# Optimization experiments

Measured on AMD Instinct MI355X. Metric: run time of the kernel, lower is better.

The kernel has to match this reference:

```python
import jax, jax.numpy as jnp
import numpy as np
import math

VOCAB, EMBED, RES = 50257, 512, 2048
B, T = 64, 512
LN_EPS = 1e-5


def setup_inputs() -> dict:
    key = jax.random.key(0)
    k_x, k_e, k_r, k_w = jax.random.split(key, 4)
    x = jax.random.randint(k_x, (B, T), 0, VOCAB)
    embed_weight = jax.random.normal(k_e, (VOCAB, EMBED), dtype=jnp.float32)
    R = jax.random.normal(k_r, (RES, RES), dtype=jnp.float32) / math.sqrt(RES) / 0.9
    Win = jax.random.normal(k_w, (EMBED, RES), dtype=jnp.float32) / math.sqrt(EMBED) / 0.9
    gamma = jnp.ones((RES,), dtype=jnp.float32)
    beta = jnp.zeros((RES,), dtype=jnp.float32)
    return {"x": x, "embed_weight": embed_weight, "R": R, "Win": Win,
            "gamma": gamma, "beta": beta}


def reference(x, embed_weight, R, Win, gamma, beta):
    emb = embed_weight[x]                              # [B, T, E]
    inp = jnp.einsum('bte,er->btr', emb, Win)          # [B, T, RES]

    def step(state, u_t):                              # state: [B, RES]
        new_state = jnp.tanh(state @ R + u_t)
        return new_state, None

    state0 = jnp.zeros((x.shape[0], R.shape[0]), dtype=emb.dtype)
    state, _ = jax.lax.scan(step, state0, jnp.swapaxes(inp, 0, 1))  # scan over T

    # LayerNorm over last dim (eps=1e-5, affine)
    mu = jnp.mean(state, axis=-1, keepdims=True)
    var = jnp.mean((state - mu) ** 2, axis=-1, keepdims=True)
    normed = (state - mu) / jnp.sqrt(var + LN_EPS)
    return normed * gamma + beta
```

## Files before the change

kernel.cpp:

```cpp
#include <hip/hip_runtime.h>

#define BB 64
#define TT 512
#define EE 512
#define RR 2048
#define CPW 32
#define RPG 16
#define NWGS 256
#define FPAD 16
#define SLOT2 (BB * RR * 2)
#define GRP2  (RPG * RR * 2)
#define SPIN_CAP (1 << 20)

typedef _Float16 f16;
typedef f16 f16x8 __attribute__((ext_vector_type(8)));
typedef float f32x4 __attribute__((ext_vector_type(4)));

__device__ __forceinline__ float fast_tanh(float v) {
  float e = __expf(2.0f * v);
  return 1.0f - 2.0f / (e + 1.0f);
}

__device__ __forceinline__ void storeS(f16* p, f16 h) {
  union { f16 h; unsigned short s; } u;
  u.h = h;
  __hip_atomic_store((unsigned short*)p, u.s, __ATOMIC_RELAXED, __HIP_MEMORY_SCOPE_AGENT);
}

__device__ __forceinline__ unsigned flag_ld(const unsigned* p) {
  return __hip_atomic_load(p, __ATOMIC_RELAXED, __HIP_MEMORY_SCOPE_AGENT);
}
__device__ __forceinline__ void flag_st(unsigned* p, unsigned v) {
  __hip_atomic_store(p, v, __ATOMIC_RELAXED, __HIP_MEMORY_SCOPE_AGENT);
}

__device__ __forceinline__ void issue8(f16x8* dst, unsigned voff, const f16* sbase) {
#pragma unroll
  for (int i = 0; i < 8; ++i)
    asm volatile("global_load_dwordx4 %0, %1, %2 offset:%c3"
                 : "=v"(dst[i]) : "v"(voff), "s"(sbase), "i"(64 * i) : "memory");
}
__device__ __forceinline__ void issue2(f16x8* dst, unsigned voff, const f16* sbase) {
  asm volatile("global_load_dwordx4 %0, %1, %2"
               : "=v"(dst[0]) : "v"(voff), "s"(sbase) : "memory");
  asm volatile("global_load_dwordx4 %0, %1, %2 offset:64"
               : "=v"(dst[1]) : "v"(voff), "s"(sbase) : "memory");
}

template <int N>
__device__ __forceinline__ void wait_vm() {
  asm volatile("s_waitcnt vmcnt(%c0)" :: "i"(N) : "memory");
  __builtin_amdgcn_sched_barrier(0);
}


__global__ void prep_emb(const int* __restrict__ x, const float* __restrict__ ew,
                         f16* __restrict__ emb) {
  const int row = blockIdx.x;
  const int tok = x[row];
  const float4* src = (const float4*)(ew + (size_t)tok * EE);
  f16* dst = emb + (size_t)row * EE;
  const int i = threadIdx.x;
  float4 v = src[i];
  union { f16 h[4]; unsigned long long u; } p;
  p.h[0] = (f16)v.x; p.h[1] = (f16)v.y; p.h[2] = (f16)v.z; p.h[3] = (f16)v.w;
  ((unsigned long long*)dst)[i] = p.u;
}

__global__ void prep_winT(const float* __restrict__ Win, f16* __restrict__ WinT) {
  const int i = blockIdx.x * blockDim.x + threadIdx.x;
  if (i < EE * RR) {
    const int k = i / RR, n = i % RR;
    WinT[(size_t)n * EE + k] = (f16)Win[i];
  }
}


__launch_bounds__(512, 1)
__global__ void scan_kernel(const float* __restrict__ R, f16* __restrict__ Sh,
                            const f16* __restrict__ emb, const f16* __restrict__ WinT,
                            unsigned* __restrict__ flg) {
  __shared__ __align__(16) char ldsbuf[CPW * RR * 2 + 16 * 1040];
  f16* Rt = (f16*)ldsbuf;
  const char* RtB = (const char*)ldsbuf;

  const int wg = blockIdx.x;
  const int xcd = wg & 7;
  const int grp = xcd >> 1;
  const int cw = ((wg >> 3) << 1) | (wg & 1);
  const int nbase = cw * CPW;
  const int rbase = grp * RPG;
  const int tid = threadIdx.x;
  const int wv = tid >> 6, l = tid & 63;
  unsigned* gflags = flg + (size_t)grp * 64 * FPAD;
  unsigned* myflag = gflags + cw * FPAD;
  f16* Sg = Sh + (size_t)grp * (RPG * RR);

  __builtin_amdgcn_fence(__ATOMIC_ACQUIRE, "agent");

  const int r16 = l & 15, kb = l >> 4;
  const int mm = tid >> 5, cc = tid & 31;
  const int ntr = cc >> 4;
  const int lred = (cc & 15) | ((mm >> 2) << 4);
  const int jred = mm & 3;
  char* red = ldsbuf + CPW * RR * 2;

  {
    const int c = tid & 31, kst = tid >> 5;
    for (int k = kst; k < RR; k += 16) {
      const float v = R[(size_t)k * RR + nbase + c];
      const int idx = ((k >> 5) << 10) + ((c >> 4) << 9) +
                      (((c & 15) << 2) + ((k >> 3) & 3)) * 8 + (k & 7);
      Rt[idx] = (f16)v;
    }
  }

  f16x8 wfr[2][2];
#pragma unroll
  for (int c2 = 0; c2 < 2; ++c2)
#pragma unroll
    for (int nt = 0; nt < 2; ++nt)
      wfr[c2][nt] = *(const f16x8*)&WinT[(size_t)(nbase + nt * 16 + r16) * EE +
                                         (2 * wv + c2) * 32 + kb * 8];

  const unsigned voffE0 =
      (unsigned)((((size_t)(rbase + r16) * TT) * EE + 2 * wv * 32 + kb * 8) * 2);

  {
    f16x8 ebuf[2];
    issue2(ebuf, voffE0 , emb);
    wait_vm<0>();
    f32x4 a0 = {0.f, 0.f, 0.f, 0.f}, a1 = {0.f, 0.f, 0.f, 0.f};
#pragma unroll
    for (int c2 = 0; c2 < 2; ++c2) {
      a0 = __builtin_amdgcn_mfma_f32_16x16x32_f16(ebuf[c2], wfr[c2][0], a0, 0, 0, 0);
      a1 = __builtin_amdgcn_mfma_f32_16x16x32_f16(ebuf[c2], wfr[c2][1], a1, 0, 0, 0);
    }
    *(f32x4*)(red + (wv * 2 + 0) * 1040 + l * 16) = a0;
    *(f32x4*)(red + (wv * 2 + 1) * 1040 + l * 16) = a1;
    __syncthreads();
    float s = 0.f;
#pragma unroll
    for (int w = 0; w < 8; ++w)
      s += *(const float*)(red + (w * 2 + ntr) * 1040 + lred * 16 + jred * 4);
    storeS(&Sg[(size_t)mm * RR + nbase + cc], (f16)fast_tanh(s));
    __syncthreads();
    if (tid == 0) flag_st(myflag, 1u);
  }

  const int kblk = (wv + cw) & 7;
  const unsigned voffA = (unsigned)(((r16 * RR) + (kblk << 8) + kb * 8) * 2);
  const int bb0 = (r16 * 4 + kb) * 16;

  f16x8 abuf[8];

  for (int tau = 2; tau <= TT; ++tau) {
    const unsigned need = (unsigned)(tau - 1);

    {
      const unsigned* pp = &gflags[(size_t)(kblk * 8 + (l & 7)) * FPAD];
      unsigned fv = flag_ld(pp);
      int gd = 0;
      while (!__all(fv >= need) && ++gd < SPIN_CAP) {
        __builtin_amdgcn_s_sleep(1);
        fv = flag_ld(pp);
      }
    }

    const f16* sprev = Sh + (size_t)(tau - 2) * (BB * RR) + (size_t)grp * (RPG * RR);
    f16* snext = (f16*)((char*)Sh + (size_t)(tau - 1) * SLOT2) + (size_t)grp * (RPG * RR);

    issue8(abuf, voffA, sprev);
    f16x8 ebuf[2];
    issue2(ebuf, voffE0 + (unsigned)((tau - 1) * (EE * 2)), emb);

    f32x4 acc0 = {0.f, 0.f, 0.f, 0.f}, acc1 = {0.f, 0.f, 0.f, 0.f};
#define KSTEP(ks)                                                              \
  {                                                                            \
    const int kc = (kblk << 3) + (ks);                                         \
    f16x8 b0 = *(const f16x8*)(RtB + kc * 2048 + bb0);                         \
    f16x8 b1 = *(const f16x8*)(RtB + kc * 2048 + 1024 + bb0);                  \
    acc0 = __builtin_amdgcn_mfma_f32_16x16x32_f16(abuf[ks], b0, acc0, 0, 0, 0);\
    acc1 = __builtin_amdgcn_mfma_f32_16x16x32_f16(abuf[ks], b1, acc1, 0, 0, 0);\
  }
    wait_vm<6>();
    KSTEP(0) KSTEP(1) KSTEP(2) KSTEP(3)
    wait_vm<2>();
    KSTEP(4) KSTEP(5) KSTEP(6) KSTEP(7)
#undef KSTEP
    wait_vm<0>();
#pragma unroll
    for (int c2 = 0; c2 < 2; ++c2) {
      acc0 = __builtin_amdgcn_mfma_f32_16x16x32_f16(ebuf[c2], wfr[c2][0], acc0, 0, 0, 0);
      acc1 = __builtin_amdgcn_mfma_f32_16x16x32_f16(ebuf[c2], wfr[c2][1], acc1, 0, 0, 0);
    }

    *(f32x4*)(red + (wv * 2 + 0) * 1040 + l * 16) = acc0;
    *(f32x4*)(red + (wv * 2 + 1) * 1040 + l * 16) = acc1;
    __syncthreads();
    {
      float s = 0.f;
#pragma unroll
      for (int w = 0; w < 8; ++w)
        s += *(const float*)(red + (w * 2 + ntr) * 1040 + lred * 16 + jred * 4);
      storeS(&snext[(size_t)mm * RR + nbase + cc], (f16)fast_tanh(s));
    }
    __syncthreads();
    if (tid == 0) flag_st(myflag, (unsigned)tau);
  }
}


__launch_bounds__(256, 1)
__global__ void ln_kernel(const char* __restrict__ slotbase, const float* __restrict__ gamma,
                          const float* __restrict__ beta, float* __restrict__ out) {
  const int b = blockIdx.x;
  const int tid = threadIdx.x;
  const f16* row = (const f16*)(slotbase + (size_t)(b >> 4) * GRP2) + (size_t)(b & 15) * RR;
  float vals[8];
  float lsum = 0.f, lsq = 0.f;
#pragma unroll
  for (int i = 0; i < 8; ++i) {
    float v = (float)row[tid + i * 256];
    vals[i] = v; lsum += v; lsq += v * v;
  }
#pragma unroll
  for (int off = 32; off >= 1; off >>= 1) {
    lsum += __shfl_xor(lsum, off);
    lsq  += __shfl_xor(lsq, off);
  }
  __shared__ float ps[4], pq[4];
  __shared__ float mu_s, rstd_s;
  const int wv = tid >> 6, l = tid & 63;
  if (l == 0) { ps[wv] = lsum; pq[wv] = lsq; }
  __syncthreads();
  if (tid == 0) {
    float s = 0.f, q = 0.f;
    for (int i = 0; i < 4; ++i) { s += ps[i]; q += pq[i]; }
    const float mu = s / RR;
    const float var = q / RR - mu * mu;
    mu_s = mu; rstd_s = rsqrtf(var + 1e-5f);
  }
  __syncthreads();
  const float mu = mu_s, rstd = rstd_s;
#pragma unroll
  for (int i = 0; i < 8; ++i) {
    const int idx = tid + i * 256;
    out[(size_t)b * RR + idx] = (vals[i] - mu) * rstd * gamma[idx] + beta[idx];
  }
}


extern "C" void kernel_launch(void* const* d_in, const int* in_sizes, int n_in,
                              void* d_out, int out_size, void* d_ws, size_t ws_size,
                              hipStream_t stream) {
  const int*   x     = (const int*)d_in[0];
  const float* ew    = (const float*)d_in[1];
  const float* Rm    = (const float*)d_in[2];
  const float* Win   = (const float*)d_in[3];
  const float* gamma = (const float*)d_in[4];
  const float* beta  = (const float*)d_in[5];

  const size_t SH_OFF  = 0;
  const size_t EMB_OFF = (size_t)TT * SLOT2;
  const size_t WT_OFF  = EMB_OFF + 33554432;
  const size_t FLG_OFF = WT_OFF + 2097152;
  const size_t NEED    = FLG_OFF + 16384;
  if (ws_size < NEED) {
    hipMemsetAsync(d_out, 0, (size_t)out_size * 4, stream);
    return;
  }
  char* ws = (char*)d_ws;
  f16*      Shist = (f16*)(ws + SH_OFF);
  f16*      emb   = (f16*)(ws + EMB_OFF);
  f16*      WinT  = (f16*)(ws + WT_OFF);
  unsigned* flg   = (unsigned*)(ws + FLG_OFF);

  hipMemsetAsync(flg, 0, 16384, stream);
  prep_emb<<<BB * TT, 128, 0, stream>>>(x, ew, emb);
  prep_winT<<<(EE * RR) / 256, 256, 0, stream>>>(Win, WinT);
  scan_kernel<<<NWGS, 512, 0, stream>>>(Rm, Shist, emb, WinT, flg);
  ln_kernel<<<BB, 256, 0, stream>>>(ws + (size_t)(TT - 1) * SLOT2,
                                    gamma, beta, (float*)d_out);
}
```

Baseline: 1.962 ms.

## Replace trailing barrier with LDS counter so one wave publishes the step flag

Removes the second __syncthreads after each step's state store. Each wave now waits for its own global stores, bumps a workgroup-scope LDS counter, and one rotating wave spins until all 8 waves have counted before setting the cross-workgroup flag. Before overwriting the reduction buffer in the next step, every wave spins on the same counter so the earlier reads are finished. The aim is to let waves start the next step's flag polling and loads without a full barrier. The cost is LDS spin loops and subtle ordering: the store-to-flag release relies on vmcnt waits plus relaxed atomics, and the uninitialized-counter race relies on the first-step barrier.

```diff
diff --git a/kernel.cpp b/kernel.cpp
--- a/kernel.cpp
+++ b/kernel.cpp
@@ -34,6 +34,13 @@
   __hip_atomic_store(p, v, __ATOMIC_RELAXED, __HIP_MEMORY_SCOPE_AGENT);
 }
 
+__device__ __forceinline__ unsigned lds_ld(const unsigned* p) {
+  return __hip_atomic_load(p, __ATOMIC_RELAXED, __HIP_MEMORY_SCOPE_WORKGROUP);
+}
+__device__ __forceinline__ void lds_add(unsigned* p) {
+  __hip_atomic_fetch_add(p, 1u, __ATOMIC_RELAXED, __HIP_MEMORY_SCOPE_WORKGROUP);
+}
+
 __device__ __forceinline__ void issue8(f16x8* dst, unsigned voff, const f16* sbase) {
 #pragma unroll
   for (int i = 0; i < 8; ++i)
@@ -81,6 +88,7 @@
                             const f16* __restrict__ emb, const f16* __restrict__ WinT,
                             unsigned* __restrict__ flg) {
   __shared__ __align__(16) char ldsbuf[CPW * RR * 2 + 16 * 1040];
+  __shared__ unsigned done;
   f16* Rt = (f16*)ldsbuf;
   const char* RtB = (const char*)ldsbuf;
 
@@ -96,6 +104,8 @@
   unsigned* myflag = gflags + cw * FPAD;
   f16* Sg = Sh + (size_t)grp * (RPG * RR);
 
+  if (tid == 0) done = 0u;
+
   __builtin_amdgcn_fence(__ATOMIC_ACQUIRE, "agent");
 
   const int r16 = l & 15, kb = l >> 4;
@@ -144,8 +154,15 @@
     for (int w = 0; w < 8; ++w)
       s += *(const float*)(red + (w * 2 + ntr) * 1040 + lred * 16 + jred * 4);
     storeS(&Sg[(size_t)mm * RR + nbase + cc], (f16)fast_tanh(s));
-    __syncthreads();
-    if (tid == 0) flag_st(myflag, 1u);
+    wait_vm<0>();
+    if (l == 0) lds_add(&done);
+    if (wv == 1) {
+      if (l == 0) {
+        unsigned d; int gd = 0;
+        do { d = lds_ld(&done); } while (d < 8u && ++gd < (1 << 22));
+        flag_st(myflag, 1u);
+      }
+    }
   }
 
   const int kblk = (wv + cw) & 7;
@@ -195,6 +212,11 @@
       acc1 = __builtin_amdgcn_mfma_f32_16x16x32_f16(ebuf[c2], wfr[c2][1], acc1, 0, 0, 0);
     }
 
+    {
+      unsigned d; int gd = 0;
+      do { d = lds_ld(&done); } while (d < 8u * (unsigned)(tau - 1) && ++gd < (1 << 22));
+    }
+
     *(f32x4*)(red + (wv * 2 + 0) * 1040 + l * 16) = acc0;
     *(f32x4*)(red + (wv * 2 + 1) * 1040 + l * 16) = acc1;
     __syncthreads();
@@ -205,8 +227,15 @@
         s += *(const float*)(red + (w * 2 + ntr) * 1040 + lred * 16 + jred * 4);
       storeS(&snext[(size_t)mm * RR + nbase + cc], (f16)fast_tanh(s));
     }
-    __syncthreads();
-    if (tid == 0) flag_st(myflag, (unsigned)tau);
+    wait_vm<0>();
+    if (l == 0) lds_add(&done);
+    if (wv == (tau & 7)) {
+      if (l == 0) {
+        unsigned d; int gd = 0;
+        do { d = lds_ld(&done); } while (d < 8u * (unsigned)tau && ++gd < (1 << 22));
+        flag_st(myflag, (unsigned)tau);
+      }
+    }
   }
 }
 
```

Result: slower. 2.316 ms (+18.0%).
